# Kernel tuning notes

Hardware: AMD Instinct MI355X
Metric: run time of the kernel (lower is better)

The kernel has to match this reference:

```python
import jax, jax.numpy as jnp
import numpy as np

N = 100000      # nodes
E = 1600000     # edges (before self loops)
F_IN = 128
HID = 128
C = 32
L = 3


def setup_inputs() -> dict:
    key = jax.random.key(0)
    k = jax.random.split(key, 7)
    x = jax.random.normal(k[0], (N, F_IN), dtype=jnp.float32)
    edge_index = jax.random.randint(k[1], (2, E), 0, N)
    norm = jax.random.uniform(k[2], (E + N,), dtype=jnp.float32)  # per-edge Jaccard norm incl. self loops
    # layer weights stored as [in, out] (equivalent to nn.Linear weight transposed)
    Ws = jax.random.normal(k[3], (L, HID, HID), dtype=jnp.float32) * (1.0 / np.sqrt(HID))
    bs = jnp.zeros((L, HID), dtype=jnp.float32)
    Wc = jax.random.normal(k[4], (HID, C), dtype=jnp.float32) * (1.0 / np.sqrt(HID))
    bc = jnp.zeros((C,), dtype=jnp.float32)
    return {"x": x, "edge_index": edge_index, "norm": norm,
            "Ws": Ws, "bs": bs, "Wc": Wc, "bc": bc}


def reference(x, edge_index, norm, Ws, bs, Wc, bc):
    n = x.shape[0]
    loops = jnp.arange(n, dtype=edge_index.dtype)
    src = jnp.concatenate([edge_index[0], loops])  # [E+N]
    dst = jnp.concatenate([edge_index[1], loops])  # [E+N]
    for i in range(L):
        h = x @ Ws[i]                               # [N, HID] linear (no bias)
        msg = norm[:, None] * h[src]                # edge-wise gather + scale
        agg = jax.ops.segment_max(msg, dst, num_segments=n)  # scatter-max
        agg = jnp.where(jnp.isneginf(agg), 0.0, agg)          # empty segments -> 0
        x = jax.nn.relu(agg + bs[i])
    logits = x @ Wc + bc
    return jax.nn.log_softmax(logits, axis=-1)
```

## Files before the change

### kernel.cpp

```cpp
#include <hip/hip_runtime.h>
#include <hip/hip_fp16.h>
#include <math.h>

#define HID 128
#define NCLS 32
#define BCAP 12288
#define SCAP 9728

typedef _Float16 half8 __attribute__((ext_vector_type(8)));
typedef _Float16 h2 __attribute__((ext_vector_type(2)));
typedef float f32x4 __attribute__((ext_vector_type(4)));

__device__ __forceinline__ void gload_lds16(const void* g, void* l) {
  __builtin_amdgcn_global_load_lds(
      (const __attribute__((address_space(1))) void*)g,
      (__attribute__((address_space(3))) void*)l, 16, 0, 0);
}

__device__ __forceinline__ h2 pk_max(h2 a, h2 b) {
  return __builtin_elementwise_max(a, b);
}

__global__ void k_prep_x(const float* __restrict__ x, __half* __restrict__ xa,
                         int total4) {
  int i = blockIdx.x * blockDim.x + threadIdx.x;
  if (i >= total4) return;
  float4 v = ((const float4*)x)[i];
  __half2* o = (__half2*)xa + i * 2;
  o[0] = __floats2half2_rn(v.x, v.y);
  o[1] = __floats2half2_rn(v.z, v.w);
}

__global__ void k_prep_w(const float* __restrict__ Ws, __half* __restrict__ Wt,
                         int total) {
  int i = blockIdx.x * blockDim.x + threadIdx.x;
  if (i >= total) return;
  int l = i >> 14, r = i & 16383;
  int nn = r >> 7, k = r & 127;
  Wt[i] = __float2half_rn(Ws[(l << 14) + k * HID + nn]);
}

__global__ __launch_bounds__(1024) void k_bin(const int* __restrict__ ei,
                                              const float* __restrict__ norm,
                                              int* __restrict__ bucket_cur,
                                              int2* __restrict__ bins,
                                              int E, int T) {
  __shared__ int bcnt[256];
  __shared__ int bbase[256];
  int tid = threadIdx.x;
  if (tid < 256) bcnt[tid] = 0;
  __syncthreads();
  int base = blockIdx.x * 8192;
  int2 ent[8];
  int bk[8];
  #pragma unroll
  for (int i = 0; i < 8; ++i) {
    int e = base + (i << 10) + tid;
    bk[i] = -1;
    if (e < T) {
      int src, dst;
      if (e < E) { src = ei[e]; dst = ei[E + e]; } else { src = dst = e - E; }
      bk[i] = dst >> 9;
      ent[i] = make_int2(src | ((dst & 511) << 17), __float_as_int(norm[e]));
      atomicAdd(&bcnt[bk[i]], 1);
    }
  }
  __syncthreads();
  if (tid < 256) {
    int c = bcnt[tid];
    bbase[tid] = c ? atomicAdd(&bucket_cur[tid], c) : 0;
    bcnt[tid] = 0;
  }
  __syncthreads();
  #pragma unroll
  for (int i = 0; i < 8; ++i) {
    if (bk[i] >= 0) {
      int pos = bbase[bk[i]] + atomicAdd(&bcnt[bk[i]], 1);
      bins[(size_t)bk[i] * BCAP + pos] = ent[i];
    }
  }
}

__global__ __launch_bounds__(256) void k_bscan(const int* __restrict__ bucket_cur,
                                               int* __restrict__ bucket_off, int nb) {
  __shared__ int a[256];
  int tid = threadIdx.x;
  int orig = (tid < nb) ? bucket_cur[tid] : 0;
  a[tid] = orig;
  __syncthreads();
  for (int d = 1; d < 256; d <<= 1) {
    int t = (tid >= d) ? a[tid - d] : 0;
    __syncthreads();
    a[tid] += t;
    __syncthreads();
  }
  if (tid < nb) bucket_off[tid] = a[tid] - orig;
  if (tid == nb - 1) bucket_off[nb] = a[tid];
}

__global__ __launch_bounds__(1024) void k_sortbucket(
    const int2* __restrict__ bins, const int* __restrict__ bucket_off,
    int2* __restrict__ csr, int* __restrict__ row_off, int n, int nb) {
  __shared__ int2 sorted[SCAP];
  __shared__ int scnt[512];
  __shared__ int wsum[8];
  int b = blockIdx.x, tid = threadIdx.x;
  int goff = bucket_off[b];
  int cnt = bucket_off[b + 1] - goff;
  if (cnt > SCAP) cnt = SCAP;
  const int2* src = bins + (size_t)b * BCAP;
  int2 myent[10];
  #pragma unroll
  for (int i = 0; i < 10; ++i) {
    int j = tid + (i << 10);
    if (j < cnt) myent[i] = src[j];
  }
  if (tid < 512) scnt[tid] = 0;
  __syncthreads();
  #pragma unroll
  for (int i = 0; i < 10; ++i) {
    int j = tid + (i << 10);
    if (j < cnt) atomicAdd(&scnt[((unsigned)myent[i].x) >> 17], 1);
  }
  __syncthreads();
  int lane = tid & 63, wid = tid >> 6;
  int v = (tid < 512) ? scnt[tid] : 0;
  int incl = v;
  #pragma unroll
  for (int d = 1; d < 64; d <<= 1) {
    int t = __shfl_up(incl, d, 64);
    if (lane >= d) incl += t;
  }
  if (tid < 512 && lane == 63) wsum[wid] = incl;
  __syncthreads();
  if (tid == 0) {
    int s = 0;
    #pragma unroll
    for (int i = 0; i < 8; ++i) { int t = wsum[i]; wsum[i] = s; s += t; }
  }
  __syncthreads();
  int excl = incl - v + ((tid < 512) ? wsum[wid] : 0);
  int node = (b << 9) + tid;
  if (tid < 512 && node < n) row_off[node] = goff + excl;
  if (b == nb - 1 && tid == 0) row_off[n] = bucket_off[nb];
  __syncthreads();
  if (tid < 512) scnt[tid] = excl;
  __syncthreads();
  #pragma unroll
  for (int i = 0; i < 10; ++i) {
    int j = tid + (i << 10);
    if (j < cnt) {
      int2 e = myent[i];
      int pos = atomicAdd(&scnt[((unsigned)e.x) >> 17], 1);
      if (pos < SCAP) sorted[pos] = make_int2(e.x & 0x1FFFF, e.y);
    }
  }
  __syncthreads();
  for (int j = tid; j < cnt; j += 1024) csr[goff + j] = sorted[j];
}

__global__ __launch_bounds__(256) void k_gemm_mfma(const __half* __restrict__ X,
                                                   const __half* __restrict__ Wl,
                                                   __half* __restrict__ H, int n) {
  __shared__ char lds[49152];
  char* ldsW = lds;
  char* ldsX = lds + 32768;
  int tid = threadIdx.x, lane = tid & 63, w = tid >> 6;
  int row0 = blockIdx.x * 64;
  int rows = n - row0; if (rows > 64) rows = 64;
  int vbytes = rows << 8;

  #pragma unroll
  for (int it = 0; it < 8; ++it) {
    int d = (w << 13) + (it << 10) + (lane << 4);
    int src = d ^ (((d >> 8) & 7) << 4);
    gload_lds16((const char*)Wl + src, ldsW + (w << 13) + (it << 10));
  }
  #pragma unroll
  for (int it = 0; it < 4; ++it) {
    int d = (w << 12) + (it << 10) + (lane << 4);
    if (d < vbytes) {
      int src = d ^ (((d >> 8) & 7) << 4);
      gload_lds16((const char*)X + ((size_t)row0 << 8) + src,
                  ldsX + (w << 12) + (it << 10));
    }
  }
  __syncthreads();

  int l15 = lane & 15, lhi = lane >> 4;
  half8 a[4];
  #pragma unroll
  for (int s = 0; s < 4; ++s) {
    int m = (w << 4) + l15;
    int d = (m << 8) + (s << 6) + (lhi << 4);
    a[s] = *(const half8*)(ldsX + (d ^ ((m & 7) << 4)));
  }
  f32x4 acc[8] = {};
  #pragma unroll
  for (int s = 0; s < 4; ++s) {
    #pragma unroll
    for (int t = 0; t < 8; ++t) {
      int nn = (t << 4) + l15;
      int d = (nn << 8) + (s << 6) + (lhi << 4);
      half8 b = *(const half8*)(ldsW + (d ^ ((nn & 7) << 4)));
      acc[t] = __builtin_amdgcn_mfma_f32_16x16x32_f16(a[s], b, acc[t], 0, 0, 0);
    }
  }
  #pragma unroll
  for (int t = 0; t < 8; ++t) {
    int col = (t << 4) + l15;
    #pragma unroll
    for (int r = 0; r < 4; ++r) {
      int row = row0 + (w << 4) + (lhi << 2) + r;
      if (row < n) H[(size_t)row * HID + col] = __float2half_rn(acc[t][r]);
    }
  }
}

__global__ __launch_bounds__(256) void k_aggregate(
    const __half* __restrict__ H, const int* __restrict__ row_off,
    const int2* __restrict__ csr, const float* __restrict__ bias,
    __half* __restrict__ Xout, int n) {
  int node = (int)((blockIdx.x * blockDim.x + threadIdx.x) >> 6);
  if (node >= n) return;
  int lane = threadIdx.x & 63;
  int q = lane >> 4, l4 = lane & 15;
  int beg = row_off[node], end = row_off[node + 1];
  const unsigned NEG = 0xFC00FC00u;
  h2 m0 = *(const h2*)&NEG, m1 = m0, m2 = m0, m3 = m0;
  int j = beg + q;
  for (; j + 4 < end; j += 8) {
    int2 e0 = csr[j];
    int2 e1 = csr[j + 4];
    _Float16 w0 = (_Float16)__int_as_float(e0.y);
    _Float16 w1 = (_Float16)__int_as_float(e1.y);
    uint4 r0 = *(const uint4*)(H + ((size_t)e0.x << 7) + (l4 << 3));
    uint4 r1 = *(const uint4*)(H + ((size_t)e1.x << 7) + (l4 << 3));
    m0 = pk_max(m0, *(h2*)&r0.x * w0);
    m1 = pk_max(m1, *(h2*)&r0.y * w0);
    m2 = pk_max(m2, *(h2*)&r0.z * w0);
    m3 = pk_max(m3, *(h2*)&r0.w * w0);
    m0 = pk_max(m0, *(h2*)&r1.x * w1);
    m1 = pk_max(m1, *(h2*)&r1.y * w1);
    m2 = pk_max(m2, *(h2*)&r1.z * w1);
    m3 = pk_max(m3, *(h2*)&r1.w * w1);
  }
  if (j < end) {
    int2 e0 = csr[j];
    _Float16 w0 = (_Float16)__int_as_float(e0.y);
    uint4 r0 = *(const uint4*)(H + ((size_t)e0.x << 7) + (l4 << 3));
    m0 = pk_max(m0, *(h2*)&r0.x * w0);
    m1 = pk_max(m1, *(h2*)&r0.y * w0);
    m2 = pk_max(m2, *(h2*)&r0.z * w0);
    m3 = pk_max(m3, *(h2*)&r0.w * w0);
  }
  #pragma unroll
  for (int d = 16; d <= 32; d <<= 1) {
    unsigned u0 = __shfl_xor(*(unsigned*)&m0, d, 64);
    unsigned u1 = __shfl_xor(*(unsigned*)&m1, d, 64);
    unsigned u2 = __shfl_xor(*(unsigned*)&m2, d, 64);
    unsigned u3 = __shfl_xor(*(unsigned*)&m3, d, 64);
    m0 = pk_max(m0, *(h2*)&u0);
    m1 = pk_max(m1, *(h2*)&u1);
    m2 = pk_max(m2, *(h2*)&u2);
    m3 = pk_max(m3, *(h2*)&u3);
  }
  if (q == 0) {
    float f0x = (float)m0.x, f0y = (float)m0.y;
    float f1x = (float)m1.x, f1y = (float)m1.y;
    float f2x = (float)m2.x, f2y = (float)m2.y;
    float f3x = (float)m3.x, f3y = (float)m3.y;
    if (end == beg) {
      f0x=f0y=f1x=f1y=f2x=f2y=f3x=f3y = 0.f;
    }
    float4 b0 = ((const float4*)bias)[l4 << 1];
    float4 b1 = ((const float4*)bias)[(l4 << 1) + 1];
    __half2 o0 = __floats2half2_rn(fmaxf(f0x + b0.x, 0.f), fmaxf(f0y + b0.y, 0.f));
    __half2 o1 = __floats2half2_rn(fmaxf(f1x + b0.z, 0.f), fmaxf(f1y + b0.w, 0.f));
    __half2 o2 = __floats2half2_rn(fmaxf(f2x + b1.x, 0.f), fmaxf(f2y + b1.y, 0.f));
    __half2 o3 = __floats2half2_rn(fmaxf(f3x + b1.z, 0.f), fmaxf(f3y + b1.w, 0.f));
    uint4 ov = make_uint4(*(unsigned*)&o0, *(unsigned*)&o1,
                          *(unsigned*)&o2, *(unsigned*)&o3);
    *(uint4*)(Xout + ((size_t)node << 7) + (l4 << 3)) = ov;
  }
}

__global__ __launch_bounds__(256) void k_classifier(
    const __half* __restrict__ X, const float* __restrict__ Wc,
    const float* __restrict__ bc, float* __restrict__ out, int n) {
  __shared__ float sW[HID * NCLS];
  __shared__ float sx[8][HID];
  int tid = threadIdx.x;
  #pragma unroll
  for (int i = 0; i < 4; ++i)
    ((float4*)sW)[tid + 256 * i] = ((const float4*)Wc)[tid + 256 * i];
  int node0 = blockIdx.x * 8;
  {
    int r = tid >> 5, c = (tid & 31) << 2;
    if (node0 + r < n) {
      __half2 p0 = *(const __half2*)&X[(size_t)(node0 + r) * HID + c];
      __half2 p1 = *(const __half2*)&X[(size_t)(node0 + r) * HID + c + 2];
      float2 f0 = __half22float2(p0), f1 = __half22float2(p1);
      sx[r][c] = f0.x; sx[r][c + 1] = f0.y; sx[r][c + 2] = f1.x; sx[r][c + 3] = f1.y;
    }
  }
  __syncthreads();
  int g = tid >> 5, c = tid & 31;
  int node = node0 + g;
  if (node >= n) return;
  float acc = bc[c];
  #pragma unroll 8
  for (int k = 0; k < HID; ++k)
    acc = fmaf(sx[g][k], sW[k * NCLS + c], acc);
  float m = acc;
  #pragma unroll
  for (int off = 16; off; off >>= 1) m = fmaxf(m, __shfl_xor(m, off, 32));
  float e = expf(acc - m);
  float s = e;
  #pragma unroll
  for (int off = 16; off; off >>= 1) s += __shfl_xor(s, off, 32);
  out[(size_t)node * NCLS + c] = acc - m - logf(s);
}

extern "C" void kernel_launch(void* const* d_in, const int* in_sizes, int n_in,
                              void* d_out, int out_size, void* d_ws, size_t ws_size,
                              hipStream_t stream) {
  const float* x    = (const float*)d_in[0];
  const int*   ei   = (const int*)d_in[1];
  const float* norm = (const float*)d_in[2];
  const float* Ws   = (const float*)d_in[3];
  const float* bs   = (const float*)d_in[4];
  const float* Wc   = (const float*)d_in[5];
  const float* bc   = (const float*)d_in[6];
  float* out = (float*)d_out;

  const int N = in_sizes[0] / HID;
  const int E = in_sizes[1] / 2;
  const int L = in_sizes[3] / (HID * HID);
  const int T = E + N;
  const int NB = (N + 511) >> 9;

  char* p = (char*)d_ws;
  auto alloc = [&](size_t bytes) {
    char* r = p; p += (bytes + 255) & ~(size_t)255; return r;
  };
  __half* xa         = (__half*)alloc((size_t)N * HID * 2);
  __half* xb         = (__half*)alloc((size_t)N * HID * 2);
  __half* hbuf       = (__half*)alloc((size_t)N * HID * 2);
  __half* Wt         = (__half*)alloc((size_t)L * HID * HID * 2);
  int*    row_off    = (int*)alloc(((size_t)N + 1) * 4);
  int*    bucket_cur = (int*)alloc(256 * 4);
  int*    bucket_off = (int*)alloc(257 * 4);
  int2*   bins       = (int2*)alloc((size_t)NB * BCAP * 8);
  int2*   csr        = (int2*)alloc((size_t)T * 8);
  (void)ws_size; (void)n_in; (void)out_size;

  hipMemsetAsync(bucket_cur, 0, 256 * 4, stream);
  k_prep_x<<<(N * 32 + 255) / 256, 256, 0, stream>>>(x, xa, N * 32);
  k_prep_w<<<(L * HID * HID + 255) / 256, 256, 0, stream>>>(Ws, Wt, L * HID * HID);
  k_bin<<<(T + 8191) / 8192, 1024, 0, stream>>>(ei, norm, bucket_cur, bins, E, T);
  k_bscan<<<1, 256, 0, stream>>>(bucket_cur, bucket_off, NB);
  k_sortbucket<<<NB, 1024, 0, stream>>>(bins, bucket_off, csr, row_off, N, NB);

  __half* xin = xa;
  __half* xout = xb;
  for (int l = 0; l < L; ++l) {
    k_gemm_mfma<<<(N + 63) / 64, 256, 0, stream>>>(
        xin, Wt + (size_t)l * HID * HID, hbuf, N);
    k_aggregate<<<(N + 3) / 4, 256, 0, stream>>>(
        hbuf, row_off, csr, bs + (size_t)l * HID, xout, N);
    __half* tmp = xin; xin = xout; xout = tmp;
  }
  k_classifier<<<(N + 7) / 8, 256, 0, stream>>>(xin, Wc, bc, out, N);
}
```

Before: 329.3 us.

## Pack CSR edges into 32-bit words and sub-sort by source slice

Each CSR entry now stores the 17-bit source index and a truncated fp16 weight in one 32-bit word, halving edge-list traffic in every aggregation pass. The bucket sort now keys on destination plus a coarse source slice, so neighbours of each node are ordered by source region for better gather cache locality. The aggregation loop keeps four edges in flight per lane group instead of two. In exchange the weight loses its lowest mantissa bit and the sort's counting and scan stages become larger.

```diff
diff --git a/kernel.cpp b/kernel.cpp
--- a/kernel.cpp
+++ b/kernel.cpp
@@ -6,10 +6,13 @@
 #define NCLS 32
 #define BCAP 12288
 #define SCAP 9728
+#define SLCSH 14
 
 typedef _Float16 half8 __attribute__((ext_vector_type(8)));
 typedef _Float16 h2 __attribute__((ext_vector_type(2)));
 typedef float f32x4 __attribute__((ext_vector_type(4)));
+
+union hbits_u { unsigned short u; _Float16 f; };
 
 __device__ __forceinline__ void gload_lds16(const void* g, void* l) {
   __builtin_amdgcn_global_load_lds(
@@ -19,6 +22,11 @@
 
 __device__ __forceinline__ h2 pk_max(h2 a, h2 b) {
   return __builtin_elementwise_max(a, b);
+}
+
+__device__ __forceinline__ _Float16 dec_w(unsigned e) {
+  hbits_u u; u.u = (unsigned short)((e >> 16) & 0xFFFEu);
+  return u.f;
 }
 
 __global__ void k_prep_x(const float* __restrict__ x, __half* __restrict__ xa,
@@ -100,63 +108,83 @@
 
 __global__ __launch_bounds__(1024) void k_sortbucket(
     const int2* __restrict__ bins, const int* __restrict__ bucket_off,
-    int2* __restrict__ csr, int* __restrict__ row_off, int n, int nb) {
-  __shared__ int2 sorted[SCAP];
-  __shared__ int scnt[512];
-  __shared__ int wsum[8];
+    unsigned* __restrict__ csr4, int* __restrict__ row_off, int n, int nb) {
+  __shared__ unsigned sorted[SCAP];
+  __shared__ int cnt_[4096];
+  __shared__ int wsum[16];
   int b = blockIdx.x, tid = threadIdx.x;
   int goff = bucket_off[b];
   int cnt = bucket_off[b + 1] - goff;
   if (cnt > SCAP) cnt = SCAP;
   const int2* src = bins + (size_t)b * BCAP;
   int2 myent[10];
+  int mykey[10];
   #pragma unroll
   for (int i = 0; i < 10; ++i) {
     int j = tid + (i << 10);
-    if (j < cnt) myent[i] = src[j];
-  }
-  if (tid < 512) scnt[tid] = 0;
+    if (j < cnt) {
+      myent[i] = src[j];
+      int s = myent[i].x & 0x1FFFF;
+      int dl = ((unsigned)myent[i].x) >> 17;
+      mykey[i] = (dl << 3) | (s >> SLCSH);
+    }
+  }
+  #pragma unroll
+  for (int i = 0; i < 4; ++i) cnt_[tid + (i << 10)] = 0;
   __syncthreads();
   #pragma unroll
   for (int i = 0; i < 10; ++i) {
     int j = tid + (i << 10);
-    if (j < cnt) atomicAdd(&scnt[((unsigned)myent[i].x) >> 17], 1);
-  }
-  __syncthreads();
+    if (j < cnt) atomicAdd(&cnt_[mykey[i]], 1);
+  }
+  __syncthreads();
+  int base = tid << 2;
+  int l0 = cnt_[base], l1 = cnt_[base + 1], l2 = cnt_[base + 2], l3 = cnt_[base + 3];
+  int s0 = l0 + l1 + l2 + l3;
   int lane = tid & 63, wid = tid >> 6;
-  int v = (tid < 512) ? scnt[tid] : 0;
-  int incl = v;
+  int incl = s0;
   #pragma unroll
   for (int d = 1; d < 64; d <<= 1) {
     int t = __shfl_up(incl, d, 64);
     if (lane >= d) incl += t;
   }
-  if (tid < 512 && lane == 63) wsum[wid] = incl;
-  __syncthreads();
-  if (tid == 0) {
-    int s = 0;
+  if (lane == 63) wsum[wid] = incl;
+  __syncthreads();
+  if (wid == 0 && lane < 16) {
+    int wv = wsum[lane];
+    int winc = wv;
     #pragma unroll
-    for (int i = 0; i < 8; ++i) { int t = wsum[i]; wsum[i] = s; s += t; }
-  }
-  __syncthreads();
-  int excl = incl - v + ((tid < 512) ? wsum[wid] : 0);
+    for (int d = 1; d < 16; d <<= 1) {
+      int t = __shfl_up(winc, d, 16);
+      if (lane >= d) winc += t;
+    }
+    wsum[lane] = winc - wv;
+  }
+  __syncthreads();
+  int excl = incl - s0 + wsum[wid];
+  cnt_[base]     = excl;
+  cnt_[base + 1] = excl + l0;
+  cnt_[base + 2] = excl + l0 + l1;
+  cnt_[base + 3] = excl + l0 + l1 + l2;
+  __syncthreads();
   int node = (b << 9) + tid;
-  if (tid < 512 && node < n) row_off[node] = goff + excl;
+  if (tid < 512 && node < n) row_off[node] = goff + cnt_[tid << 3];
   if (b == nb - 1 && tid == 0) row_off[n] = bucket_off[nb];
-  __syncthreads();
-  if (tid < 512) scnt[tid] = excl;
   __syncthreads();
   #pragma unroll
   for (int i = 0; i < 10; ++i) {
     int j = tid + (i << 10);
     if (j < cnt) {
-      int2 e = myent[i];
-      int pos = atomicAdd(&scnt[((unsigned)e.x) >> 17], 1);
-      if (pos < SCAP) sorted[pos] = make_int2(e.x & 0x1FFFF, e.y);
-    }
-  }
-  __syncthreads();
-  for (int j = tid; j < cnt; j += 1024) csr[goff + j] = sorted[j];
+      int pos = atomicAdd(&cnt_[mykey[i]], 1);
+      if (pos < SCAP) {
+        __half h = __float2half_rn(__int_as_float(myent[i].y));
+        unsigned short hb = *(unsigned short*)&h;
+        sorted[pos] = (unsigned)(myent[i].x & 0x1FFFF) | ((unsigned)(hb >> 1) << 17);
+      }
+    }
+  }
+  __syncthreads();
+  for (int j = tid; j < cnt; j += 1024) csr4[goff + j] = sorted[j];
 }
 
 __global__ __launch_bounds__(256) void k_gemm_mfma(const __half* __restrict__ X,
@@ -219,23 +247,24 @@
 
 __global__ __launch_bounds__(256) void k_aggregate(
     const __half* __restrict__ H, const int* __restrict__ row_off,
-    const int2* __restrict__ csr, const float* __restrict__ bias,
+    const unsigned* __restrict__ csr4, const float* __restrict__ bias,
     __half* __restrict__ Xout, int n) {
   int node = (int)((blockIdx.x * blockDim.x + threadIdx.x) >> 6);
   if (node >= n) return;
   int lane = threadIdx.x & 63;
   int q = lane >> 4, l4 = lane & 15;
   int beg = row_off[node], end = row_off[node + 1];
+  const char* Hb = (const char*)H + (l4 << 4);
   const unsigned NEG = 0xFC00FC00u;
   h2 m0 = *(const h2*)&NEG, m1 = m0, m2 = m0, m3 = m0;
   int j = beg + q;
-  for (; j + 4 < end; j += 8) {
-    int2 e0 = csr[j];
-    int2 e1 = csr[j + 4];
-    _Float16 w0 = (_Float16)__int_as_float(e0.y);
-    _Float16 w1 = (_Float16)__int_as_float(e1.y);
-    uint4 r0 = *(const uint4*)(H + ((size_t)e0.x << 7) + (l4 << 3));
-    uint4 r1 = *(const uint4*)(H + ((size_t)e1.x << 7) + (l4 << 3));
+  for (; j + 12 < end; j += 16) {
+    unsigned e0 = csr4[j], e1 = csr4[j + 4], e2 = csr4[j + 8], e3 = csr4[j + 12];
+    _Float16 w0 = dec_w(e0), w1 = dec_w(e1), w2 = dec_w(e2), w3 = dec_w(e3);
+    uint4 r0 = *(const uint4*)(Hb + ((size_t)(e0 & 0x1FFFF) << 8));
+    uint4 r1 = *(const uint4*)(Hb + ((size_t)(e1 & 0x1FFFF) << 8));
+    uint4 r2 = *(const uint4*)(Hb + ((size_t)(e2 & 0x1FFFF) << 8));
+    uint4 r3 = *(const uint4*)(Hb + ((size_t)(e3 & 0x1FFFF) << 8));
     m0 = pk_max(m0, *(h2*)&r0.x * w0);
     m1 = pk_max(m1, *(h2*)&r0.y * w0);
     m2 = pk_max(m2, *(h2*)&r0.z * w0);
@@ -244,11 +273,19 @@
     m1 = pk_max(m1, *(h2*)&r1.y * w1);
     m2 = pk_max(m2, *(h2*)&r1.z * w1);
     m3 = pk_max(m3, *(h2*)&r1.w * w1);
-  }
-  if (j < end) {
-    int2 e0 = csr[j];
-    _Float16 w0 = (_Float16)__int_as_float(e0.y);
-    uint4 r0 = *(const uint4*)(H + ((size_t)e0.x << 7) + (l4 << 3));
+    m0 = pk_max(m0, *(h2*)&r2.x * w2);
+    m1 = pk_max(m1, *(h2*)&r2.y * w2);
+    m2 = pk_max(m2, *(h2*)&r2.z * w2);
+    m3 = pk_max(m3, *(h2*)&r2.w * w2);
+    m0 = pk_max(m0, *(h2*)&r3.x * w3);
+    m1 = pk_max(m1, *(h2*)&r3.y * w3);
+    m2 = pk_max(m2, *(h2*)&r3.z * w3);
+    m3 = pk_max(m3, *(h2*)&r3.w * w3);
+  }
+  for (; j < end; j += 4) {
+    unsigned e0 = csr4[j];
+    _Float16 w0 = dec_w(e0);
+    uint4 r0 = *(const uint4*)(Hb + ((size_t)(e0 & 0x1FFFF) << 8));
     m0 = pk_max(m0, *(h2*)&r0.x * w0);
     m1 = pk_max(m1, *(h2*)&r0.y * w0);
     m2 = pk_max(m2, *(h2*)&r0.z * w0);
@@ -281,7 +318,7 @@
     __half2 o3 = __floats2half2_rn(fmaxf(f3x + b1.z, 0.f), fmaxf(f3y + b1.w, 0.f));
     uint4 ov = make_uint4(*(unsigned*)&o0, *(unsigned*)&o1,
                           *(unsigned*)&o2, *(unsigned*)&o3);
-    *(uint4*)(Xout + ((size_t)node << 7) + (l4 << 3)) = ov;
+    *(uint4*)((char*)Xout + ((size_t)node << 8) + (l4 << 4)) = ov;
   }
 }
 
@@ -344,15 +381,15 @@
   auto alloc = [&](size_t bytes) {
     char* r = p; p += (bytes + 255) & ~(size_t)255; return r;
   };
-  __half* xa         = (__half*)alloc((size_t)N * HID * 2);
-  __half* xb         = (__half*)alloc((size_t)N * HID * 2);
-  __half* hbuf       = (__half*)alloc((size_t)N * HID * 2);
-  __half* Wt         = (__half*)alloc((size_t)L * HID * HID * 2);
-  int*    row_off    = (int*)alloc(((size_t)N + 1) * 4);
-  int*    bucket_cur = (int*)alloc(256 * 4);
-  int*    bucket_off = (int*)alloc(257 * 4);
-  int2*   bins       = (int2*)alloc((size_t)NB * BCAP * 8);
-  int2*   csr        = (int2*)alloc((size_t)T * 8);
+  __half*   xa         = (__half*)alloc((size_t)N * HID * 2);
+  __half*   xb         = (__half*)alloc((size_t)N * HID * 2);
+  __half*   hbuf       = (__half*)alloc((size_t)N * HID * 2);
+  __half*   Wt         = (__half*)alloc((size_t)L * HID * HID * 2);
+  int*      row_off    = (int*)alloc(((size_t)N + 1) * 4);
+  int*      bucket_cur = (int*)alloc(256 * 4);
+  int*      bucket_off = (int*)alloc(257 * 4);
+  int2*     bins       = (int2*)alloc((size_t)NB * BCAP * 8);
+  unsigned* csr4       = (unsigned*)alloc((size_t)T * 4);
   (void)ws_size; (void)n_in; (void)out_size;
 
   hipMemsetAsync(bucket_cur, 0, 256 * 4, stream);
@@ -360,7 +397,7 @@
   k_prep_w<<<(L * HID * HID + 255) / 256, 256, 0, stream>>>(Ws, Wt, L * HID * HID);
   k_bin<<<(T + 8191) / 8192, 1024, 0, stream>>>(ei, norm, bucket_cur, bins, E, T);
   k_bscan<<<1, 256, 0, stream>>>(bucket_cur, bucket_off, NB);
-  k_sortbucket<<<NB, 1024, 0, stream>>>(bins, bucket_off, csr, row_off, N, NB);
+  k_sortbucket<<<NB, 1024, 0, stream>>>(bins, bucket_off, csr4, row_off, N, NB);
 
   __half* xin = xa;
   __half* xout = xb;
@@ -368,7 +405,7 @@
     k_gemm_mfma<<<(N + 63) / 64, 256, 0, stream>>>(
         xin, Wt + (size_t)l * HID * HID, hbuf, N);
     k_aggregate<<<(N + 3) / 4, 256, 0, stream>>>(
-        hbuf, row_off, csr, bs + (size_t)l * HID, xout, N);
+        hbuf, row_off, csr4, bs + (size_t)l * HID, xout, N);
     __half* tmp = xin; xin = xout; xout = tmp;
   }
   k_classifier<<<(N + 7) / 8, 256, 0, stream>>>(xin, Wc, bc, out, N);
```

Result: no change. 324.2 us (-1.6%).
